# Performance work log

Hardware: AMD Instinct MI355X
Metric: run time of the kernel (lower is better)

Reference implementation:

```python
import jax, jax.numpy as jnp
import numpy as np

N_NODES = 100000
D = 40


def sgconv(x, src, dst, W, b, n_nodes):
    """PyG SGConv with K=1: symmetric gcn_norm with self-loops, then linear."""
    # add self loops
    loop = jnp.arange(n_nodes, dtype=src.dtype)
    s = jnp.concatenate([src, loop])
    d = jnp.concatenate([dst, loop])
    ones = jnp.ones(s.shape[0], dtype=x.dtype)
    deg = jax.ops.segment_sum(ones, d, num_segments=n_nodes)
    dinv = jnp.where(deg > 0, jax.lax.rsqrt(deg), 0.0)
    norm = dinv[s] * dinv[d]                      # [E+N]
    msg = norm[:, None] * x[s]                    # gather + scale, [E+N, D]
    agg = jax.ops.segment_sum(msg, d, num_segments=n_nodes)  # scatter-add, [N, D]
    return agg @ W.T + b


def setup_inputs() -> dict:
    key = jax.random.key(0)
    k1, k2, k3, k4, k5, k6 = jax.random.split(key, 6)
    x = jax.random.normal(k1, (N_NODES, D), dtype=jnp.float32)
    edge_index = jax.random.randint(k2, (2, 1600000), 0, N_NODES, dtype=jnp.int64)
    s = 1.0 / np.sqrt(D)
    W1 = jax.random.uniform(k3, (D, D), jnp.float32, -s, s)
    b1 = jax.random.uniform(k4, (D,), jnp.float32, -s, s)
    W2 = jax.random.uniform(k5, (D, D), jnp.float32, -s, s)
    b2 = jax.random.uniform(k6, (D,), jnp.float32, -s, s)
    return {"x": x, "edge_index": edge_index, "W1": W1, "b1": b1, "W2": W2, "b2": b2}


def reference(x, edge_index, W1, b1, W2, b2):
    src, dst = edge_index[0], edge_index[1]
    n = x.shape[0]
    h = jax.nn.relu(sgconv(x, src, dst, W1, b1, n))
    out = sgconv(h, src, dst, W2, b2, n)
    return out.reshape(n * out.shape[1])  # generalizes x.view(1600)
```

## Files before the change

### kernel.cpp

```cpp
#include <hip/hip_runtime.h>
#include <hip/hip_fp16.h>

#define DD 40
#define PITER 32
#define NP 512
#define SROW_LD 44

__global__ void k_binA(const int* __restrict__ src, const int* __restrict__ dst,
                       int* __restrict__ gcur, unsigned* __restrict__ ebin,
                       int E, int PS, unsigned M, int CAPB) {
  __shared__ int hist[NP];
  __shared__ int curs[NP];
  const int tid = threadIdx.x;
  hist[tid] = 0;
  hist[tid + 256] = 0;
  __syncthreads();
  const int base = blockIdx.x * (256 * PITER);
  for (int it = 0; it < PITER; ++it) {
    int i = base + it * 256 + tid;
    if (i < E) {
      unsigned t = (unsigned)dst[i];
      int b = (int)(((unsigned long long)t * M) >> 31);
      atomicAdd(&hist[b], 1);
    }
  }
  __syncthreads();
#pragma unroll
  for (int q = 0; q < 2; ++q) {
    int b = tid + q * 256;
    int h = hist[b];
    int old = h ? atomicAdd(&gcur[b], h) : 0;
    curs[b] = b * CAPB + old;
  }
  __syncthreads();
  for (int it = 0; it < PITER; ++it) {
    int i = base + it * 256 + tid;
    if (i < E) {
      unsigned t = (unsigned)dst[i];
      int b = (int)(((unsigned long long)t * M) >> 31);
      unsigned local = t - (unsigned)(b * PS);
      int pos = atomicAdd(&curs[b], 1);
      ebin[pos] = (local << 17) | (unsigned)src[i];
    }
  }
}

__global__ __launch_bounds__(256) void k_partB(
    const unsigned* __restrict__ ebin, const int* __restrict__ gcur,
    int* __restrict__ ideg, int* __restrict__ cursor, float* __restrict__ dinv,
    int* __restrict__ es, int PS, int CAPB, int CAPE, int n) {
  __shared__ int sdeg[256];
  __shared__ int sbuf[2][256];
  __shared__ int scur[256];
  const int p = blockIdx.x;
  const int tid = threadIdx.x;
  const int start = p * CAPB;
  const int cnt = gcur[p];

  sdeg[tid] = 0;
  __syncthreads();
  for (int i = tid; i < cnt; i += 256) atomicAdd(&sdeg[ebin[start + i] >> 17], 1);
  __syncthreads();

  int v = sdeg[tid];
  sbuf[0][tid] = v;
  __syncthreads();
  int pi = 0;
  for (int off = 1; off < 256; off <<= 1) {
    int x = sbuf[pi][tid];
    if (tid >= off) x += sbuf[pi][tid - off];
    sbuf[pi ^ 1][tid] = x;
    __syncthreads();
    pi ^= 1;
  }
  int incl = sbuf[pi][tid];
  scur[tid] = incl - v;

  const int node = p * PS + tid;
  if (tid < PS && node < n) {
    ideg[node] = v;
    cursor[node] = p * CAPE + incl;
    dinv[node] = rsqrtf((float)(v + 1));
  }
  __syncthreads();

  for (int i = tid; i < cnt; i += 256) {
    unsigned pk = ebin[start + i];
    int l = (int)(pk >> 17);
    int pos = atomicAdd(&scur[l], 1);
    es[p * CAPE + pos] = (int)(pk & 0x1FFFFu);
  }
}

__global__ void k_prescale(const float4* __restrict__ x4, const float* __restrict__ dinv,
                           uint2* __restrict__ xs8, int n4) {
  int i = blockIdx.x * blockDim.x + threadIdx.x;
  if (i < n4) {
    float w = dinv[i / 10];
    float4 v = x4[i];
    __half2 ha = __float22half2_rn(make_float2(v.x * w, v.y * w));
    __half2 hb = __float22half2_rn(make_float2(v.z * w, v.w * w));
    uint2 u;
    u.x = *(unsigned*)&ha;
    u.y = *(unsigned*)&hb;
    xs8[i] = u;
  }
}

template <int OUT_HALF>
__global__ __launch_bounds__(256) void k_layer(
    const uint4* __restrict__ in4, const int* __restrict__ es,
    const int* __restrict__ ideg, const int* __restrict__ cursor,
    const float* __restrict__ dinv, const float* __restrict__ W,
    const float* __restrict__ bias, float* __restrict__ outf,
    __half2* __restrict__ outh, int n) {
  __shared__ float sWT[DD * DD];
  __shared__ float sb[DD];
  __shared__ float srow[48][SROW_LD];
  const int tid = threadIdx.x;

  const int w = tid >> 6, lane = tid & 63;
  const int g = lane / 5, pos = lane - g * 5;
  const int v = blockIdx.x * 48 + w * 12 + g;

#define ACC8(U, A)                                   \
  {                                                  \
    const __half2* hh = (const __half2*)&(U);        \
    float2 f0 = __half22float2(hh[0]);               \
    float2 f1 = __half22float2(hh[1]);               \
    float2 f2 = __half22float2(hh[2]);               \
    float2 f3 = __half22float2(hh[3]);               \
    A[0] += f0.x; A[1] += f0.y; A[2] += f1.x;        \
    A[3] += f1.y; A[4] += f2.x; A[5] += f2.y;        \
    A[6] += f3.x; A[7] += f3.y;                      \
  }

  if (g < 12 && v < n) {
    const int e1 = cursor[v];
    int e = e1 - ideg[v];
    float a[8], b[8];
    {
      uint4 u = in4[(size_t)v * 5 + pos];
      const __half2* hh = (const __half2*)&u;
      float2 f0 = __half22float2(hh[0]);
      float2 f1 = __half22float2(hh[1]);
      float2 f2 = __half22float2(hh[2]);
      float2 f3 = __half22float2(hh[3]);
      a[0] = f0.x; a[1] = f0.y; a[2] = f1.x; a[3] = f1.y;
      a[4] = f2.x; a[5] = f2.y; a[6] = f3.x; a[7] = f3.y;
#pragma unroll
      for (int q = 0; q < 8; ++q) b[q] = 0.f;
    }
    for (; e + 7 < e1; e += 8) {
      int s0 = es[e],     s1 = es[e + 1], s2 = es[e + 2], s3 = es[e + 3];
      int s4 = es[e + 4], s5 = es[e + 5], s6 = es[e + 6], s7 = es[e + 7];
      uint4 u0 = in4[(size_t)s0 * 5 + pos];
      uint4 u1 = in4[(size_t)s1 * 5 + pos];
      uint4 u2 = in4[(size_t)s2 * 5 + pos];
      uint4 u3 = in4[(size_t)s3 * 5 + pos];
      uint4 u4 = in4[(size_t)s4 * 5 + pos];
      uint4 u5 = in4[(size_t)s5 * 5 + pos];
      uint4 u6 = in4[(size_t)s6 * 5 + pos];
      uint4 u7 = in4[(size_t)s7 * 5 + pos];
      ACC8(u0, a); ACC8(u1, b); ACC8(u2, a); ACC8(u3, b);
      ACC8(u4, a); ACC8(u5, b); ACC8(u6, a); ACC8(u7, b);
    }
    for (; e + 3 < e1; e += 4) {
      int s0 = es[e], s1 = es[e + 1], s2 = es[e + 2], s3 = es[e + 3];
      uint4 u0 = in4[(size_t)s0 * 5 + pos];
      uint4 u1 = in4[(size_t)s1 * 5 + pos];
      uint4 u2 = in4[(size_t)s2 * 5 + pos];
      uint4 u3 = in4[(size_t)s3 * 5 + pos];
      ACC8(u0, a); ACC8(u1, b); ACC8(u2, a); ACC8(u3, b);
    }
    for (; e < e1; ++e) {
      uint4 uu = in4[(size_t)es[e] * 5 + pos];
      ACC8(uu, a);
    }
    float* r = &srow[w * 12 + g][pos * 8];
#pragma unroll
    for (int q = 0; q < 8; ++q) r[q] = a[q] + b[q];
  }

  for (int t = tid; t < DD * DD; t += 256) sWT[(t % DD) * DD + t / DD] = W[t];
  if (tid < DD) sb[tid] = bias[tid];
  __syncthreads();

  if (OUT_HALF) {
    for (int i = tid; i < 48 * 20; i += 256) {
      int l = i / 20, jj = i - l * 20;
      int vv = blockIdx.x * 48 + l;
      if (vv < n) {
        float dv = dinv[vv];
        const float* row = srow[l];
        float s0 = 0.f, s1 = 0.f;
#pragma unroll
        for (int k = 0; k < DD; ++k) {
          s0 = fmaf(row[k], sWT[k * DD + 2 * jj], s0);
          s1 = fmaf(row[k], sWT[k * DD + 2 * jj + 1], s1);
        }
        s0 = fmaf(s0, dv, sb[2 * jj]);
        s1 = fmaf(s1, dv, sb[2 * jj + 1]);
        s0 = fmaxf(s0, 0.f) * dv;
        s1 = fmaxf(s1, 0.f) * dv;
        outh[(size_t)vv * 20 + jj] = __float22half2_rn(make_float2(s0, s1));
      }
    }
  } else {
    for (int i = tid; i < 48 * DD; i += 256) {
      int l = i / DD, j = i - l * DD;
      int vv = blockIdx.x * 48 + l;
      if (vv < n) {
        float dv = dinv[vv];
        const float* row = srow[l];
        float acc = 0.f;
#pragma unroll
        for (int k = 0; k < DD; ++k) acc = fmaf(row[k], sWT[k * DD + j], acc);
        outf[(size_t)vv * DD + j] = fmaf(acc, dv, sb[j]);
      }
    }
  }
#undef ACC8
}

extern "C" void kernel_launch(void* const* d_in, const int* in_sizes, int n_in,
                              void* d_out, int out_size, void* d_ws, size_t ws_size,
                              hipStream_t stream) {
  const float* x = (const float*)d_in[0];
  const int* ei = (const int*)d_in[1];
  const float* W1 = (const float*)d_in[2];
  const float* b1 = (const float*)d_in[3];
  const float* W2 = (const float*)d_in[4];
  const float* b2 = (const float*)d_in[5];

  const int n = in_sizes[0] / DD;
  const int E = in_sizes[1] / 2;
  const int* src = ei;
  const int* dst = ei + E;
  const int n4 = n * (DD / 4);
  const int PS = (n + NP - 1) / NP;
  const unsigned M = (unsigned)((((unsigned long long)1 << 31) + PS - 1) / PS);
  const int CAPB = E / NP + 512;
  const int CAPE = CAPB;
  const int NCH = (E + 256 * PITER - 1) / (256 * PITER);

  float* out = (float*)d_out;

  char* w = (char*)d_ws;
  float* dinv = (float*)w;   w += (size_t)n * 4;
  int* ideg = (int*)w;       w += (size_t)n * 4;
  int* cursor = (int*)w;     w += (size_t)n * 4;
  int* gcur = (int*)w;       w += (size_t)NP * 4;
  char* ebin_hs = w;         w += (size_t)n * DD * 2;
  int* es = (int*)w;         w += (size_t)NP * CAPE * 4;
  uint2* xs8 = (uint2*)w;    w += (size_t)n * DD * 2;

  unsigned* ebin = (unsigned*)ebin_hs;
  uint2* hs8 = (uint2*)ebin_hs;

  hipMemsetAsync(gcur, 0, (size_t)NP * 4, stream);

  k_binA<<<NCH, 256, 0, stream>>>(src, dst, gcur, ebin, E, PS, M, CAPB);
  k_partB<<<NP, 256, 0, stream>>>(ebin, gcur, ideg, cursor, dinv, es, PS, CAPB, CAPE, n);
  k_prescale<<<(n4 + 255) / 256, 256, 0, stream>>>((const float4*)x, dinv, xs8, n4);

  const int NBK = (n + 47) / 48;
  k_layer<1><<<NBK, 256, 0, stream>>>((const uint4*)xs8, es, ideg, cursor, dinv, W1, b1,
                                      nullptr, (__half2*)hs8, n);
  k_layer<0><<<NBK, 256, 0, stream>>>((const uint4*)hs8, es, ideg, cursor, dinv, W2, b2,
                                      out, nullptr, n);
}
```

Before: 151.8 us.

## Sort nodes by degree within partitions, prefetch edge indices, pad weight LDS

```diff
diff --git a/kernel.cpp b/kernel.cpp
--- a/kernel.cpp
+++ b/kernel.cpp
@@ -2,9 +2,10 @@
 #include <hip/hip_fp16.h>
 
 #define DD 40
-#define PITER 32
+#define PITER 8
 #define NP 512
 #define SROW_LD 44
+#define SWT_LD 41
 
 __global__ void k_binA(const int* __restrict__ src, const int* __restrict__ dst,
                        int* __restrict__ gcur, unsigned* __restrict__ ebin,
@@ -48,16 +49,20 @@
 __global__ __launch_bounds__(256) void k_partB(
     const unsigned* __restrict__ ebin, const int* __restrict__ gcur,
     int* __restrict__ ideg, int* __restrict__ cursor, float* __restrict__ dinv,
-    int* __restrict__ es, int PS, int CAPB, int CAPE, int n) {
+    int* __restrict__ es, int* __restrict__ nodeord,
+    int PS, int CAPB, int CAPE, int n) {
   __shared__ int sdeg[256];
   __shared__ int sbuf[2][256];
   __shared__ int scur[256];
+  __shared__ int dh[64];
   const int p = blockIdx.x;
   const int tid = threadIdx.x;
   const int start = p * CAPB;
   const int cnt = gcur[p];
 
   sdeg[tid] = 0;
+  if (tid < 64) dh[tid] = 0;
+  if (tid < PS) nodeord[p * PS + tid] = -1;
   __syncthreads();
   for (int i = tid; i < cnt; i += 256) atomicAdd(&sdeg[ebin[start + i] >> 17], 1);
   __syncthreads();
@@ -77,12 +82,25 @@
   scur[tid] = incl - v;
 
   const int node = p * PS + tid;
-  if (tid < PS && node < n) {
+  const int isnode = (tid < PS && node < n);
+  const int dc = min(v, 63);
+  if (isnode) {
     ideg[node] = v;
     cursor[node] = p * CAPE + incl;
     dinv[node] = rsqrtf((float)(v + 1));
-  }
-  __syncthreads();
+    atomicAdd(&dh[dc], 1);
+  }
+  __syncthreads();
+
+  if (tid == 0) {
+    int s = 0;
+    for (int q = 0; q < 64; ++q) { int h = dh[q]; dh[q] = s; s += h; }
+  }
+  __syncthreads();
+  if (isnode) {
+    int r = atomicAdd(&dh[dc], 1);
+    nodeord[p * PS + r] = node;
+  }
 
   for (int i = tid; i < cnt; i += 256) {
     unsigned pk = ebin[start + i];
@@ -111,17 +129,24 @@
 __global__ __launch_bounds__(256) void k_layer(
     const uint4* __restrict__ in4, const int* __restrict__ es,
     const int* __restrict__ ideg, const int* __restrict__ cursor,
-    const float* __restrict__ dinv, const float* __restrict__ W,
-    const float* __restrict__ bias, float* __restrict__ outf,
-    __half2* __restrict__ outh, int n) {
-  __shared__ float sWT[DD * DD];
+    const float* __restrict__ dinv, const int* __restrict__ nodeord,
+    const float* __restrict__ W, const float* __restrict__ bias,
+    float* __restrict__ outf, __half2* __restrict__ outh, int nslots) {
+  __shared__ float sWT[DD * SWT_LD];
   __shared__ float sb[DD];
   __shared__ float srow[48][SROW_LD];
+  __shared__ int svnode[48];
   const int tid = threadIdx.x;
+
+  if (tid < 48) {
+    int slot = blockIdx.x * 48 + tid;
+    svnode[tid] = (slot < nslots) ? nodeord[slot] : -1;
+  }
+  __syncthreads();
 
   const int w = tid >> 6, lane = tid & 63;
   const int g = lane / 5, pos = lane - g * 5;
-  const int v = blockIdx.x * 48 + w * 12 + g;
+  const int v = (g < 12) ? svnode[w * 12 + g] : -1;
 
 #define ACC8(U, A)                                   \
   {                                                  \
@@ -135,7 +160,7 @@
     A[6] += f3.x; A[7] += f3.y;                      \
   }
 
-  if (g < 12 && v < n) {
+  if (v >= 0) {
     const int e1 = cursor[v];
     int e = e1 - ideg[v];
     float a[8], b[8];
@@ -151,9 +176,20 @@
 #pragma unroll
       for (int q = 0; q < 8; ++q) b[q] = 0.f;
     }
-    for (; e + 7 < e1; e += 8) {
-      int s0 = es[e],     s1 = es[e + 1], s2 = es[e + 2], s3 = es[e + 3];
-      int s4 = es[e + 4], s5 = es[e + 5], s6 = es[e + 6], s7 = es[e + 7];
+    int n0, n1, n2, n3, n4, n5, n6, n7;
+    bool have = (e + 7 < e1);
+    if (have) {
+      n0 = es[e];     n1 = es[e + 1]; n2 = es[e + 2]; n3 = es[e + 3];
+      n4 = es[e + 4]; n5 = es[e + 5]; n6 = es[e + 6]; n7 = es[e + 7];
+    }
+    while (have) {
+      int s0 = n0, s1 = n1, s2 = n2, s3 = n3, s4 = n4, s5 = n5, s6 = n6, s7 = n7;
+      int en = e + 8;
+      have = (en + 7 < e1);
+      if (have) {
+        n0 = es[en];     n1 = es[en + 1]; n2 = es[en + 2]; n3 = es[en + 3];
+        n4 = es[en + 4]; n5 = es[en + 5]; n6 = es[en + 6]; n7 = es[en + 7];
+      }
       uint4 u0 = in4[(size_t)s0 * 5 + pos];
       uint4 u1 = in4[(size_t)s1 * 5 + pos];
       uint4 u2 = in4[(size_t)s2 * 5 + pos];
@@ -164,6 +200,7 @@
       uint4 u7 = in4[(size_t)s7 * 5 + pos];
       ACC8(u0, a); ACC8(u1, b); ACC8(u2, a); ACC8(u3, b);
       ACC8(u4, a); ACC8(u5, b); ACC8(u6, a); ACC8(u7, b);
+      e = en;
     }
     for (; e + 3 < e1; e += 4) {
       int s0 = es[e], s1 = es[e + 1], s2 = es[e + 2], s3 = es[e + 3];
@@ -182,22 +219,22 @@
     for (int q = 0; q < 8; ++q) r[q] = a[q] + b[q];
   }
 
-  for (int t = tid; t < DD * DD; t += 256) sWT[(t % DD) * DD + t / DD] = W[t];
+  for (int t = tid; t < DD * DD; t += 256) sWT[(t % DD) * SWT_LD + t / DD] = W[t];
   if (tid < DD) sb[tid] = bias[tid];
   __syncthreads();
 
   if (OUT_HALF) {
     for (int i = tid; i < 48 * 20; i += 256) {
       int l = i / 20, jj = i - l * 20;
-      int vv = blockIdx.x * 48 + l;
-      if (vv < n) {
+      int vv = svnode[l];
+      if (vv >= 0) {
         float dv = dinv[vv];
         const float* row = srow[l];
         float s0 = 0.f, s1 = 0.f;
 #pragma unroll
         for (int k = 0; k < DD; ++k) {
-          s0 = fmaf(row[k], sWT[k * DD + 2 * jj], s0);
-          s1 = fmaf(row[k], sWT[k * DD + 2 * jj + 1], s1);
+          s0 = fmaf(row[k], sWT[k * SWT_LD + 2 * jj], s0);
+          s1 = fmaf(row[k], sWT[k * SWT_LD + 2 * jj + 1], s1);
         }
         s0 = fmaf(s0, dv, sb[2 * jj]);
         s1 = fmaf(s1, dv, sb[2 * jj + 1]);
@@ -209,13 +246,13 @@
   } else {
     for (int i = tid; i < 48 * DD; i += 256) {
       int l = i / DD, j = i - l * DD;
-      int vv = blockIdx.x * 48 + l;
-      if (vv < n) {
+      int vv = svnode[l];
+      if (vv >= 0) {
         float dv = dinv[vv];
         const float* row = srow[l];
         float acc = 0.f;
 #pragma unroll
-        for (int k = 0; k < DD; ++k) acc = fmaf(row[k], sWT[k * DD + j], acc);
+        for (int k = 0; k < DD; ++k) acc = fmaf(row[k], sWT[k * SWT_LD + j], acc);
         outf[(size_t)vv * DD + j] = fmaf(acc, dv, sb[j]);
       }
     }
@@ -243,6 +280,7 @@
   const int CAPB = E / NP + 512;
   const int CAPE = CAPB;
   const int NCH = (E + 256 * PITER - 1) / (256 * PITER);
+  const int NSLOT = NP * PS;
 
   float* out = (float*)d_out;
 
@@ -251,6 +289,7 @@
   int* ideg = (int*)w;       w += (size_t)n * 4;
   int* cursor = (int*)w;     w += (size_t)n * 4;
   int* gcur = (int*)w;       w += (size_t)NP * 4;
+  int* nodeord = (int*)w;    w += (size_t)NSLOT * 4;
   char* ebin_hs = w;         w += (size_t)n * DD * 2;
   int* es = (int*)w;         w += (size_t)NP * CAPE * 4;
   uint2* xs8 = (uint2*)w;    w += (size_t)n * DD * 2;
@@ -261,12 +300,13 @@
   hipMemsetAsync(gcur, 0, (size_t)NP * 4, stream);
 
   k_binA<<<NCH, 256, 0, stream>>>(src, dst, gcur, ebin, E, PS, M, CAPB);
-  k_partB<<<NP, 256, 0, stream>>>(ebin, gcur, ideg, cursor, dinv, es, PS, CAPB, CAPE, n);
+  k_partB<<<NP, 256, 0, stream>>>(ebin, gcur, ideg, cursor, dinv, es, nodeord,
+                                  PS, CAPB, CAPE, n);
   k_prescale<<<(n4 + 255) / 256, 256, 0, stream>>>((const float4*)x, dinv, xs8, n4);
 
-  const int NBK = (n + 47) / 48;
-  k_layer<1><<<NBK, 256, 0, stream>>>((const uint4*)xs8, es, ideg, cursor, dinv, W1, b1,
-                                      nullptr, (__half2*)hs8, n);
-  k_layer<0><<<NBK, 256, 0, stream>>>((const uint4*)hs8, es, ideg, cursor, dinv, W2, b2,
-                                      out, nullptr, n);
-}
+  const int NBK = (NSLOT + 47) / 48;
+  k_layer<1><<<NBK, 256, 0, stream>>>((const uint4*)xs8, es, ideg, cursor, dinv, nodeord,
+                                      W1, b1, nullptr, (__half2*)hs8, NSLOT);
+  k_layer<0><<<NBK, 256, 0, stream>>>((const uint4*)hs8, es, ideg, cursor, dinv, nodeord,
+                                      W2, b2, out, nullptr, NSLOT);
+}
```

New measurement: 162.1 us. 6.7% more time.
